# Kernel optimization log

Hardware: AMD Instinct MI355X
Metric: run time of the kernel (lower is better)

Reference implementation:

```python
import jax, jax.numpy as jnp
import numpy as np

HEADS = 16

def setup_inputs() -> dict:
    key = jax.random.key(0)
    k1, k2, k3 = jax.random.split(key, 3)
    B, S, D = 4, 2048, 1024
    x = jax.random.normal(k1, (B, S, D), dtype=jnp.float32)
    w_qkv = jax.random.normal(k2, (D, 3 * D), dtype=jnp.float32) * (D ** -0.5)
    w_out = jax.random.normal(k3, (D, D), dtype=jnp.float32) * (D ** -0.5)
    return {"x": x, "w_qkv": w_qkv, "w_out": w_out}

def reference(x, w_qkv, w_out):
    B, S, D = x.shape
    H = HEADS
    hd = D // H
    qkv = jnp.einsum("bsd,de->bse", x, w_qkv)  # [B,S,3D]
    q, k, v = jnp.split(qkv, 3, axis=-1)
    # [B,S,D] -> [B,H,S,hd]
    q = q.reshape(B, S, H, hd).transpose(0, 2, 1, 3)
    k = k.reshape(B, S, H, hd).transpose(0, 2, 1, 3)
    v = v.reshape(B, S, H, hd).transpose(0, 2, 1, 3)
    scores = jnp.einsum("bhqd,bhkd->bhqk", q, k) / jnp.sqrt(jnp.float32(hd))
    attn = jax.nn.softmax(scores, axis=-1)
    out = jnp.einsum("bhqk,bhkd->bhqd", attn, v)  # [B,H,S,hd]
    out = out.transpose(0, 2, 1, 3).reshape(B, S, D)
    return jnp.einsum("bsd,de->bse", out, w_out)
```

## Files before the change

kernel.cpp:

```cpp
#include <hip/hip_runtime.h>

typedef __bf16 bf16;
typedef __bf16 bfx8 __attribute__((ext_vector_type(8)));
typedef __bf16 bfx4 __attribute__((ext_vector_type(4)));
typedef float f32x4 __attribute__((ext_vector_type(4)));

#define MFMA_BF16 __builtin_amdgcn_mfma_f32_16x16x32_bf16

static constexpr int Bq = 4, Sq = 2048, Dq = 1024, Hq = 16, HDq = 64;
static constexpr int Mq = Bq * Sq;
static constexpr int D3 = 3 * Dq;
static constexpr float L2E = 1.4426950408889634f;
static constexpr float QSC = 0.125f * L2E;

typedef const __attribute__((address_space(1))) void* gas1;
typedef __attribute__((address_space(3))) void* las3;

__device__ __forceinline__ void gload_lds16(const bf16* g, bf16* l) {
    __builtin_amdgcn_global_load_lds((gas1)g, (las3)l, 16, 0, 0);
}

__device__ __forceinline__ float fast_exp2(float x) {
    return __builtin_amdgcn_exp2f(x);
}

__global__ __launch_bounds__(256) void cast_f32_bf16(const float* __restrict__ in,
                                                     bf16* __restrict__ out, int n) {
    int i = (blockIdx.x * 256 + threadIdx.x) * 4;
    if (i + 3 < n) {
        float4 v = *(const float4*)(in + i);
        bfx4 r;
        r[0] = (bf16)v.x; r[1] = (bf16)v.y; r[2] = (bf16)v.z; r[3] = (bf16)v.w;
        *(bfx4*)(out + i) = r;
    }
}

__global__ __launch_bounds__(256) void transpose_cast(const float* __restrict__ in,
                                                      bf16* __restrict__ out, int R, int C) {
    __shared__ float tile[32][33];
    int tx = threadIdx.x, ty = threadIdx.y;
    int c0 = blockIdx.x * 32, r0 = blockIdx.y * 32;
    for (int j = 0; j < 32; j += 8)
        tile[ty + j][tx] = in[(size_t)(r0 + ty + j) * C + c0 + tx];
    __syncthreads();
    for (int j = 0; j < 32; j += 8)
        out[(size_t)(c0 + ty + j) * R + r0 + tx] = (bf16)tile[tx][ty + j];
}

__global__ __launch_bounds__(256) void vtrans(const bf16* __restrict__ qkv,
                                              bf16* __restrict__ Vt) {
    __shared__ bf16 tile[32][33];
    int tx = threadIdx.x, ty = threadIdx.y;
    int c0 = blockIdx.x * 32;
    int s0 = blockIdx.y * 32;
    int b = blockIdx.z;
    for (int j = 0; j < 32; j += 8)
        tile[ty + j][tx] = qkv[(size_t)(b * Sq + s0 + ty + j) * D3 + 2 * Dq + c0 + tx];
    __syncthreads();
    for (int j = 0; j < 32; j += 8)
        Vt[((size_t)b * Dq + c0 + ty + j) * Sq + s0 + tx] = tile[tx][ty + j];
}

template <bool OUT_F32, bool QSCALE>
__global__ __launch_bounds__(256) void gemm_bt(const bf16* __restrict__ A,
                                               const bf16* __restrict__ Bt,
                                               void* __restrict__ Cout,
                                               int M, int N, int K) {
    __shared__ bf16 As[128 * 64];
    __shared__ bf16 Bs[128 * 64];
    int m0 = blockIdx.y * 128;
    int n0 = blockIdx.x * 128;
    int tid = threadIdx.x;
    int lane = tid & 63, wave = tid >> 6;
    int quad = lane >> 4, l16 = lane & 15;
    int wr = wave >> 1, wc = wave & 1;
    int sw = l16 & 7;

    f32x4 acc[4][4] = {};

    for (int k0 = 0; k0 < K; k0 += 64) {
        __syncthreads();
        #pragma unroll
        for (int i = 0; i < 4; i++) {
            int c = i * 256 + tid;
            int row = c >> 3;
            int ch = (c & 7) ^ (row & 7);
            gload_lds16(A + (size_t)(m0 + row) * K + k0 + ch * 8, As + c * 8);
            gload_lds16(Bt + (size_t)(n0 + row) * K + k0 + ch * 8, Bs + c * 8);
        }
        __syncthreads();
        #pragma unroll
        for (int s = 0; s < 2; s++) {
            bfx8 af[4], bfr[4];
            #pragma unroll
            for (int i = 0; i < 4; i++)
                af[i] = *(const bfx8*)(As + (wr * 64 + i * 16 + l16) * 64 +
                                       ((s * 4 + quad) ^ sw) * 8);
            #pragma unroll
            for (int j = 0; j < 4; j++)
                bfr[j] = *(const bfx8*)(Bs + (wc * 64 + j * 16 + l16) * 64 +
                                        ((s * 4 + quad) ^ sw) * 8);
            #pragma unroll
            for (int i = 0; i < 4; i++)
                #pragma unroll
                for (int j = 0; j < 4; j++)
                    acc[i][j] = MFMA_BF16(af[i], bfr[j], acc[i][j], 0, 0, 0);
        }
    }

    #pragma unroll
    for (int i = 0; i < 4; i++)
        #pragma unroll
        for (int j = 0; j < 4; j++) {
            int col = n0 + wc * 64 + j * 16 + l16;
            float scale = (QSCALE && col < Dq) ? QSC : 1.0f;
            #pragma unroll
            for (int r = 0; r < 4; r++) {
                int row = m0 + wr * 64 + i * 16 + quad * 4 + r;
                if (OUT_F32)
                    ((float*)Cout)[(size_t)row * N + col] = acc[i][j][r];
                else
                    ((bf16*)Cout)[(size_t)row * N + col] = (bf16)(acc[i][j][r] * scale);
            }
        }
}

__global__ __launch_bounds__(256, 4) void attn_kernel(const bf16* __restrict__ qkv,
                                                      const bf16* __restrict__ Vt,
                                                      bf16* __restrict__ out) {
    __shared__ bf16 Ks[2][64 * 64];
    __shared__ bf16 Vs[2][64 * 64];
    __shared__ bf16 Ps[4][32 * 32];

    int bid = blockIdx.x;
    int qc = (bid >> 3) & 15;
    int head = ((bid >> 7) << 3) | (bid & 7);
    int h = head & 15, b = head >> 4;
    int tid = threadIdx.x;
    int lane = tid & 63, wave = tid >> 6;
    int quad = lane >> 4, l16 = lane & 15;
    int sw = l16 & 7;
    int sw4 = l16 & 3;

    size_t base = (size_t)b * Sq * D3;
    const bf16* Kbase = qkv + base + Dq + h * HDq;
    const bf16* Vbase = Vt + ((size_t)b * Dq + h * HDq) * Sq;
    int q0 = qc * 128 + wave * 32;

    bfx8 qf[2][2];
    #pragma unroll
    for (int qt = 0; qt < 2; qt++)
        #pragma unroll
        for (int s = 0; s < 2; s++)
            qf[qt][s] = *(const bfx8*)(qkv + base + (size_t)(q0 + qt * 16 + l16) * D3 +
                                       h * HDq + s * 32 + quad * 8);

    bfx8 ones;
    #pragma unroll
    for (int j = 0; j < 8; j++) ones[j] = (bf16)1.0f;

    f32x4 oacc[2][4] = {};
    f32x4 lacc[2] = {};

    int c0 = tid, c1 = tid + 256;
    int r0 = c0 >> 3, ch0 = (c0 & 7) ^ (r0 & 7);
    int r1 = c1 >> 3, ch1 = (c1 & 7) ^ (r1 & 7);

    gload_lds16(Kbase + (size_t)r0 * D3 + ch0 * 8, Ks[0] + c0 * 8);
    gload_lds16(Vbase + (size_t)r0 * Sq + ch0 * 8, Vs[0] + c0 * 8);
    gload_lds16(Kbase + (size_t)r1 * D3 + ch1 * 8, Ks[0] + c1 * 8);
    gload_lds16(Vbase + (size_t)r1 * Sq + ch1 * 8, Vs[0] + c1 * 8);

    for (int i = 0; i < 32; i++) {
        int cur = i & 1;
        __syncthreads();
        if (i + 1 < 32) {
            int k0 = (i + 1) * 64;
            bf16* kd = Ks[cur ^ 1];
            bf16* vd = Vs[cur ^ 1];
            gload_lds16(Kbase + (size_t)(k0 + r0) * D3 + ch0 * 8, kd + c0 * 8);
            gload_lds16(Vbase + (size_t)r0 * Sq + k0 + ch0 * 8, vd + c0 * 8);
            gload_lds16(Kbase + (size_t)(k0 + r1) * D3 + ch1 * 8, kd + c1 * 8);
            gload_lds16(Vbase + (size_t)r1 * Sq + k0 + ch1 * 8, vd + c1 * 8);
        }
        const bf16* K_ = Ks[cur];
        const bf16* V_ = Vs[cur];

        #pragma unroll
        for (int hf = 0; hf < 2; hf++) {
            bfx8 kf[2][2];
            #pragma unroll
            for (int tp = 0; tp < 2; tp++) {
                int krow = ((2 * hf + tp) * 16 + l16) * 64;
                kf[tp][0] = *(const bfx8*)(K_ + krow + (quad ^ sw) * 8);
                kf[tp][1] = *(const bfx8*)(K_ + krow + ((4 + quad) ^ sw) * 8);
            }

            #pragma unroll
            for (int qt = 0; qt < 2; qt++) {
                f32x4 s[2] = {};
                #pragma unroll
                for (int tp = 0; tp < 2; tp++) {
                    s[tp] = MFMA_BF16(kf[tp][0], qf[qt][0], s[tp], 0, 0, 0);
                    s[tp] = MFMA_BF16(kf[tp][1], qf[qt][1], s[tp], 0, 0, 0);
                }
                #pragma unroll
                for (int tp = 0; tp < 2; tp++) {
                    bfx4 pk;
                    #pragma unroll
                    for (int r = 0; r < 4; r++)
                        pk[r] = (bf16)fast_exp2(s[tp][r]);
                    int slot = (2 * tp + (quad >> 1)) ^ sw4;
                    *(bfx4*)(&Ps[wave][(qt * 16 + l16) * 32 + slot * 8 + (quad & 1) * 4]) = pk;
                }
            }

            bfx8 pf[2];
            #pragma unroll
            for (int qt = 0; qt < 2; qt++) {
                pf[qt] = *(const bfx8*)(&Ps[wave][(qt * 16 + l16) * 32 + (quad ^ sw4) * 8]);
                lacc[qt] = MFMA_BF16(pf[qt], ones, lacc[qt], 0, 0, 0);
            }

            #pragma unroll
            for (int nt = 0; nt < 4; nt++) {
                bfx8 vf = *(const bfx8*)(V_ + (nt * 16 + l16) * 64 +
                                         ((hf * 4 + quad) ^ sw) * 8);
                #pragma unroll
                for (int qt = 0; qt < 2; qt++)
                    oacc[qt][nt] = MFMA_BF16(pf[qt], vf, oacc[qt][nt], 0, 0, 0);
            }
        }
    }

    #pragma unroll
    for (int qt = 0; qt < 2; qt++)
        #pragma unroll
        for (int r = 0; r < 4; r++) {
            int row = q0 + qt * 16 + quad * 4 + r;
            float inv = 1.0f / lacc[qt][r];
            #pragma unroll
            for (int nt = 0; nt < 4; nt++)
                out[((size_t)b * Sq + row) * Dq + h * HDq + nt * 16 + l16] =
                    (bf16)(oacc[qt][nt][r] * inv);
        }
}

extern "C" void kernel_launch(void* const* d_in, const int* in_sizes, int n_in,
                              void* d_out, int out_size, void* d_ws, size_t ws_size,
                              hipStream_t stream) {
    const float* x     = (const float*)d_in[0];
    const float* w_qkv = (const float*)d_in[1];
    const float* w_out = (const float*)d_in[2];
    float* out = (float*)d_out;

    char* ws = (char*)d_ws;
    bf16* x_bf   = (bf16*)ws;
    bf16* wqkvT  = (bf16*)(ws + 16777216);
    bf16* woutT  = (bf16*)(ws + 16777216 + 6291456);
    bf16* qkv    = (bf16*)(ws + 16777216 + 6291456 + 2097152);
    bf16* attn   = (bf16*)(ws + 16777216 + 6291456 + 2097152 + 50331648);
    bf16* Vt     = x_bf;

    cast_f32_bf16<<<(Mq * Dq) / 4 / 256, 256, 0, stream>>>(x, x_bf, Mq * Dq);
    dim3 tb(32, 8);
    transpose_cast<<<dim3(D3 / 32, Dq / 32), tb, 0, stream>>>(w_qkv, wqkvT, Dq, D3);
    transpose_cast<<<dim3(Dq / 32, Dq / 32), tb, 0, stream>>>(w_out, woutT, Dq, Dq);

    gemm_bt<false, true><<<dim3(D3 / 128, Mq / 128), 256, 0, stream>>>(x_bf, wqkvT, qkv, Mq, D3, Dq);

    vtrans<<<dim3(Dq / 32, Sq / 32, Bq), tb, 0, stream>>>(qkv, Vt);

    attn_kernel<<<1024, 256, 0, stream>>>(qkv, Vt, attn);

    gemm_bt<true, false><<<dim3(Dq / 128, Mq / 128), 256, 0, stream>>>(attn, woutT, out, Mq, Dq, Dq);
}
```

Baseline: 266.8 us.

## Keep softmax probabilities in registers and use 16x16x16 MFMA for PV

Removes the per-wave LDS staging of exponentiated scores. Because the S^T output layout of the QK MFMA matches the B-operand layout of the 16x16x16 bf16 MFMA, P now feeds the PV product straight from registers. The row-sum is accumulated in fp32 registers and reduced with cross-lane shuffles at the end, which replaces the extra MFMA against a ones vector. This drops LDS writes, reads and a dependency stall, but doubles the number of PV MFMA instructions because the narrower-K variant is used, and it raises register pressure.

New measurement: 292.5 us. +9.6%, slower.

```diff
diff --git a/kernel.cpp b/kernel.cpp
--- a/kernel.cpp
+++ b/kernel.cpp
@@ -3,6 +3,7 @@
 typedef __bf16 bf16;
 typedef __bf16 bfx8 __attribute__((ext_vector_type(8)));
 typedef __bf16 bfx4 __attribute__((ext_vector_type(4)));
+typedef short sx4 __attribute__((ext_vector_type(4)));
 typedef float f32x4 __attribute__((ext_vector_type(4)));
 
 #define MFMA_BF16 __builtin_amdgcn_mfma_f32_16x16x32_bf16
@@ -22,6 +23,11 @@
 
 __device__ __forceinline__ float fast_exp2(float x) {
     return __builtin_amdgcn_exp2f(x);
+}
+
+__device__ __forceinline__ f32x4 mfma16(bfx4 a, bfx4 b, f32x4 c) {
+    return __builtin_amdgcn_mfma_f32_16x16x16bf16_1k(
+        __builtin_bit_cast(sx4, a), __builtin_bit_cast(sx4, b), c, 0, 0, 0);
 }
 
 __global__ __launch_bounds__(256) void cast_f32_bf16(const float* __restrict__ in,
@@ -130,7 +136,6 @@
                                                       bf16* __restrict__ out) {
     __shared__ bf16 Ks[2][64 * 64];
     __shared__ bf16 Vs[2][64 * 64];
-    __shared__ bf16 Ps[4][32 * 32];
 
     int bid = blockIdx.x;
     int qc = (bid >> 3) & 15;
@@ -140,7 +145,6 @@
     int lane = tid & 63, wave = tid >> 6;
     int quad = lane >> 4, l16 = lane & 15;
     int sw = l16 & 7;
-    int sw4 = l16 & 3;
 
     size_t base = (size_t)b * Sq * D3;
     const bf16* Kbase = qkv + base + Dq + h * HDq;
@@ -155,12 +159,8 @@
             qf[qt][s] = *(const bfx8*)(qkv + base + (size_t)(q0 + qt * 16 + l16) * D3 +
                                        h * HDq + s * 32 + quad * 8);
 
-    bfx8 ones;
-    #pragma unroll
-    for (int j = 0; j < 8; j++) ones[j] = (bf16)1.0f;
-
     f32x4 oacc[2][4] = {};
-    f32x4 lacc[2] = {};
+    float lsum[2] = {0.f, 0.f};
 
     int c0 = tid, c1 = tid + 256;
     int r0 = c0 >> 3, ch0 = (c0 & 7) ^ (r0 & 7);
@@ -186,51 +186,49 @@
         const bf16* K_ = Ks[cur];
         const bf16* V_ = Vs[cur];
 
-        #pragma unroll
-        for (int hf = 0; hf < 2; hf++) {
-            bfx8 kf[2][2];
-            #pragma unroll
-            for (int tp = 0; tp < 2; tp++) {
-                int krow = ((2 * hf + tp) * 16 + l16) * 64;
-                kf[tp][0] = *(const bfx8*)(K_ + krow + (quad ^ sw) * 8);
-                kf[tp][1] = *(const bfx8*)(K_ + krow + ((4 + quad) ^ sw) * 8);
+        bfx4 pk[2][4];
+        #pragma unroll
+        for (int t = 0; t < 4; t++) {
+            bfx8 kf0 = *(const bfx8*)(K_ + (t * 16 + l16) * 64 + (quad ^ sw) * 8);
+            bfx8 kf1 = *(const bfx8*)(K_ + (t * 16 + l16) * 64 + ((4 + quad) ^ sw) * 8);
+            #pragma unroll
+            for (int qt = 0; qt < 2; qt++) {
+                f32x4 s = {};
+                s = MFMA_BF16(kf0, qf[qt][0], s, 0, 0, 0);
+                s = MFMA_BF16(kf1, qf[qt][1], s, 0, 0, 0);
+                bfx4 p;
+                float a = 0.f;
+                #pragma unroll
+                for (int r = 0; r < 4; r++) {
+                    float e = fast_exp2(s[r]);
+                    p[r] = (bf16)e;
+                    a += e;
+                }
+                pk[qt][t] = p;
+                lsum[qt] += a;
             }
-
-            #pragma unroll
-            for (int qt = 0; qt < 2; qt++) {
-                f32x4 s[2] = {};
-                #pragma unroll
-                for (int tp = 0; tp < 2; tp++) {
-                    s[tp] = MFMA_BF16(kf[tp][0], qf[qt][0], s[tp], 0, 0, 0);
-                    s[tp] = MFMA_BF16(kf[tp][1], qf[qt][1], s[tp], 0, 0, 0);
-                }
-                #pragma unroll
-                for (int tp = 0; tp < 2; tp++) {
-                    bfx4 pk;
-                    #pragma unroll
-                    for (int r = 0; r < 4; r++)
-                        pk[r] = (bf16)fast_exp2(s[tp][r]);
-                    int slot = (2 * tp + (quad >> 1)) ^ sw4;
-                    *(bfx4*)(&Ps[wave][(qt * 16 + l16) * 32 + slot * 8 + (quad & 1) * 4]) = pk;
-                }
-            }
-
-            bfx8 pf[2];
-            #pragma unroll
-            for (int qt = 0; qt < 2; qt++) {
-                pf[qt] = *(const bfx8*)(&Ps[wave][(qt * 16 + l16) * 32 + (quad ^ sw4) * 8]);
-                lacc[qt] = MFMA_BF16(pf[qt], ones, lacc[qt], 0, 0, 0);
-            }
-
-            #pragma unroll
-            for (int nt = 0; nt < 4; nt++) {
-                bfx8 vf = *(const bfx8*)(V_ + (nt * 16 + l16) * 64 +
-                                         ((hf * 4 + quad) ^ sw) * 8);
+        }
+
+        #pragma unroll
+        for (int nt = 0; nt < 4; nt++) {
+            #pragma unroll
+            for (int t = 0; t < 4; t++) {
+                bfx4 vf = *(const bfx4*)(V_ + (nt * 16 + l16) * 64 +
+                                         ((2 * t + (quad >> 1)) ^ sw) * 8 + 4 * (quad & 1));
                 #pragma unroll
                 for (int qt = 0; qt < 2; qt++)
-                    oacc[qt][nt] = MFMA_BF16(pf[qt], vf, oacc[qt][nt], 0, 0, 0);
+                    oacc[qt][nt] = mfma16(pk[qt][t], vf, oacc[qt][nt]);
             }
         }
+    }
+
+    float lfull[2];
+    #pragma unroll
+    for (int qt = 0; qt < 2; qt++) {
+        float v = lsum[qt];
+        v += __shfl_xor(v, 16);
+        v += __shfl_xor(v, 32);
+        lfull[qt] = v;
     }
 
     #pragma unroll
@@ -238,7 +236,7 @@
         #pragma unroll
         for (int r = 0; r < 4; r++) {
             int row = q0 + qt * 16 + quad * 4 + r;
-            float inv = 1.0f / lacc[qt][r];
+            float inv = 1.0f / __shfl(lfull[qt], quad * 4 + r);
             #pragma unroll
             for (int nt = 0; nt < 4; nt++)
                 out[((size_t)b * Sq + row) * Dq + h * HDq + nt * 16 + l16] =
```
